# Performance work log

Hardware: AMD Instinct MI355X
Metric: run time of the kernel (lower is better)

## Reference

```python
import jax, jax.numpy as jnp
import numpy as np

DIM = 128
WIN = (2, 7, 7)
HEADS = 4
N = WIN[0] * WIN[1] * WIN[2]  # 98
B_ = 2048
NW = 256  # num windows per sample; B_ // NW = batch = 8


def _relative_position_index(win):
    t = np.arange(win[0]); h = np.arange(win[1]); w = np.arange(win[2])
    coords = np.stack(np.meshgrid(t, h, w, indexing='ij'))  # (3, T, H, W)
    cf = coords.reshape(3, -1)  # (3, N)
    rel = cf[:, :, None] - cf[:, None, :]  # (3, N, N)
    rel = rel.transpose(1, 2, 0).copy()
    rel[:, :, 0] += win[0] - 1
    rel[:, :, 1] += win[1] - 1
    rel[:, :, 2] += win[2] - 1
    rel[:, :, 0] *= (2 * win[1] - 1) * (2 * win[2] - 1)
    rel[:, :, 1] *= 2 * win[2] - 1
    return rel.sum(-1).astype(np.int32)  # (N, N)


def setup_inputs() -> dict:
    key = jax.random.key(0)
    ks = jax.random.split(key, 8)
    table_len = (2 * WIN[0] - 1) * (2 * WIN[1] - 1) * (2 * WIN[2] - 1)  # 507
    x = jax.random.normal(ks[0], (B_, N, DIM), dtype=jnp.float32)
    # 0 / -inf style additive mask (use -1e4 as finite -inf)
    u = jax.random.uniform(ks[1], (NW, N, N))
    mask = jnp.where(u < 0.9, 0.0, -1e4).astype(jnp.float32)
    qkv_w = jax.random.normal(ks[2], (3 * DIM, DIM), dtype=jnp.float32) * (DIM ** -0.5)
    qkv_b = jax.random.normal(ks[3], (3 * DIM,), dtype=jnp.float32) * 0.02
    proj_w = jax.random.normal(ks[4], (DIM, DIM), dtype=jnp.float32) * (DIM ** -0.5)
    proj_b = jax.random.normal(ks[5], (DIM,), dtype=jnp.float32) * 0.02
    bias_table = jax.random.normal(ks[6], (table_len, HEADS), dtype=jnp.float32) * 0.02
    rel_index = jnp.asarray(_relative_position_index(WIN))
    return {"x": x, "mask": mask, "qkv_w": qkv_w, "qkv_b": qkv_b,
            "proj_w": proj_w, "proj_b": proj_b, "bias_table": bias_table,
            "rel_index": rel_index}


def reference(x, mask, qkv_w, qkv_b, proj_w, proj_b, bias_table, rel_index):
    Bq, n, c = x.shape
    hd = c // HEADS
    scale = hd ** -0.5
    qkv = x @ qkv_w.T + qkv_b  # (B_, N, 3C)
    qkv = qkv.reshape(Bq, n, 3, HEADS, hd).transpose(2, 0, 3, 1, 4)  # (3, B_, H, N, hd)
    q, k, v = qkv[0] * scale, qkv[1], qkv[2]
    attn = jnp.einsum('bhnd,bhmd->bhnm', q, k)  # (B_, H, N, N)
    bias = bias_table[rel_index.reshape(-1)].reshape(n, n, HEADS)
    attn = attn + bias.transpose(2, 0, 1)[None]  # add (1, H, N, N)
    nW = mask.shape[0]
    attn = attn.reshape(Bq // nW, nW, HEADS, n, n) + mask[None, :, None]
    attn = jax.nn.softmax(attn.reshape(Bq, HEADS, n, n), axis=-1)
    out = jnp.einsum('bhnm,bhmd->bhnd', attn, v)  # (B_, H, N, hd)
    out = out.transpose(0, 2, 1, 3).reshape(Bq, n, c)
    return out @ proj_w.T + proj_b
```

## Files before the change

### kernel.cpp

```cpp
#include <hip/hip_runtime.h>
#include <hip/hip_bf16.h>


#define NTOK 98
#define NN (NTOK * NTOK)
#define SCALE 0.17677669529663687f
#define LOG2E 1.4426950408889634f

typedef short bf16x8 __attribute__((ext_vector_type(8)));
typedef float f32x4 __attribute__((ext_vector_type(4)));
#define MFMA(a, b, c) __builtin_amdgcn_mfma_f32_16x16x32_bf16(a, b, c, 0, 0, 0)

static __device__ __forceinline__ unsigned short f2bf(float f) {
  union { float f; unsigned int i; } x; x.f = f;
  unsigned int u = x.i;
  unsigned int rnd = ((u >> 16) & 1u) + 0x7fffu;
  return (unsigned short)((u + rnd) >> 16);
}

static __device__ __forceinline__ unsigned int cvt_pk_bf16(float lo, float hi) {
  unsigned int pk;
  asm("v_cvt_pk_bf16_f32 %0, %1, %2" : "=v"(pk) : "v"(lo), "v"(hi));
  return pk;
}

__global__ void k0_w(const float* __restrict__ qkv_w, const float* __restrict__ proj_w,
                     unsigned short* __restrict__ wqb, unsigned short* __restrict__ wpb) {
  int idx = blockIdx.x * 256 + threadIdx.x;
  if (idx < 49152) wqb[idx] = f2bf(qkv_w[idx]);
  else wpb[idx - 49152] = f2bf(proj_w[idx - 49152]);
}

__global__ void k0b_bm(const float* __restrict__ table, const int* __restrict__ rel,
                       const float* __restrict__ mask, unsigned int* __restrict__ bm) {
  const int wmodh = blockIdx.x, mt = blockIdx.y;
  const int wmod = wmodh >> 2, h = wmodh & 3;
  unsigned int* dst = bm + (size_t)(wmodh * 7 + mt) * 896;
  for (int u = threadIdx.x; u < 896; u += 256) {
    int w = u & 1, lane = (u >> 1) & 63, nt = u >> 7;
    int quad = lane >> 4, L15 = lane & 15;
    int col = nt * 16 + L15;
    unsigned int pk = 0;
#pragma unroll
    for (int rr = 0; rr < 2; ++rr) {
      int row = mt * 16 + quad * 4 + 2 * w + rr;
      float v = -1.0e30f;
      if (row < NTOK && col < NTOK) {
        int nm = row * NTOK + col;
        v = (table[rel[nm] * 4 + h] + mask[(size_t)wmod * NN + nm]) * LOG2E;
      }
      pk |= ((unsigned int)f2bf(v)) << (16 * rr);
    }
    dst[u] = pk;
  }
}

__global__ __launch_bounds__(256) void k1_qkv(const float* __restrict__ x,
                                              const unsigned short* __restrict__ wqb,
                                              const float* __restrict__ qkv_b,
                                              unsigned short* __restrict__ q,
                                              unsigned short* __restrict__ k,
                                              unsigned short* __restrict__ v) {
  __shared__ unsigned short xt[64 * 136];
  __shared__ unsigned short wt[128 * 136];
  const int t = threadIdx.x;
  const int r0 = blockIdx.x * 64;
  const int wv = t >> 6, lane = t & 63, L15 = lane & 15, quad = lane >> 4;

#pragma unroll
  for (int i = 0; i < 8; ++i) {
    int idx = t + (i << 8);
    int row = idx >> 5, c4 = idx & 31;
    float4 xv = *(const float4*)&x[(size_t)(r0 + row) * 128 + c4 * 4];
    ushort4 pk; pk.x = f2bf(xv.x); pk.y = f2bf(xv.y); pk.z = f2bf(xv.z); pk.w = f2bf(xv.w);
    *(ushort4*)&xt[row * 136 + c4 * 4] = pk;
  }

  bf16x8 af[4];
  bool afLoaded = false;

  for (int g = 0; g < 3; ++g) {
    if (g) __syncthreads();
#pragma unroll
    for (int i = 0; i < 8; ++i) {
      int idx = t + (i << 8);
      int c = idx >> 4, kq = idx & 15;
      *(uint4*)&wt[c * 136 + kq * 8] = ((const uint4*)wqb)[g * 2048 + idx];
    }
    __syncthreads();
    if (!afLoaded) {
      afLoaded = true;
#pragma unroll
      for (int kt = 0; kt < 4; ++kt)
        af[kt] = *(const bf16x8*)&xt[(wv * 16 + L15) * 136 + kt * 32 + quad * 8];
    }

    f32x4 acc[8];
#pragma unroll
    for (int nt = 0; nt < 8; ++nt) {
      f32x4 a = {0.f, 0.f, 0.f, 0.f};
#pragma unroll
      for (int kt = 0; kt < 4; ++kt) {
        bf16x8 bf_ = *(const bf16x8*)&wt[(nt * 16 + L15) * 136 + kt * 32 + quad * 8];
        a = MFMA(af[kt], bf_, a);
      }
      acc[nt] = a;
    }

    unsigned short* dst = (g == 0) ? q : ((g == 1) ? k : v);
    const float sc = (g == 0) ? (SCALE * LOG2E) : 1.0f;
    float bsc[8];
#pragma unroll
    for (int nt = 0; nt < 8; ++nt) bsc[nt] = qkv_b[g * 128 + nt * 16 + L15] * sc;
#pragma unroll
    for (int reg = 0; reg < 4; ++reg) {
      int R = r0 + wv * 16 + quad * 4 + reg;
      int b = R / NTOK, n = R - b * NTOK;
      size_t base0 = ((size_t)b * 4 * NTOK + n) * 32;
#pragma unroll
      for (int h2 = 0; h2 < 4; ++h2) {
        float v0 = acc[2 * h2][reg] * sc + bsc[2 * h2];
        float v1 = acc[2 * h2 + 1][reg] * sc + bsc[2 * h2 + 1];
        unsigned int pk = cvt_pk_bf16(v0, v1);
        unsigned short* dp = dst + base0 + (size_t)h2 * (NTOK * 32) + L15;
        dp[0]  = (unsigned short)pk;
        dp[16] = (unsigned short)(pk >> 16);
      }
    }
  }
}

__global__ __launch_bounds__(256, 4) void k2_attn(const unsigned short* __restrict__ qg,
                                                  const unsigned short* __restrict__ kg,
                                                  const unsigned short* __restrict__ vg,
                                                  const unsigned int* __restrict__ bm16,
                                                  unsigned short* __restrict__ og) {
  __shared__ unsigned short sK[112 * 40];
  __shared__ unsigned short sVt[32 * 136];
  __shared__ unsigned short sP[4 * 16 * 136];
  const int t = threadIdx.x;
  const int wmodh = blockIdx.x;
  const int wmod = wmodh >> 2, h = wmodh & 3;
  const int wv = t >> 6, lane = t & 63, L15 = lane & 15, quad = lane >> 4;
  unsigned short* myP = sP + wv * (16 * 136);

  for (int i = t; i < 280; i += 256) ((unsigned int*)sK)[1960 + i] = 0;
  for (int j = lane; j < 128; j += 64) {
    int r = j >> 3, cp = j & 7;
    *(unsigned int*)&myP[r * 136 + 112 + cp * 2] = 0;
  }
  for (int i = t; i < 32 * 30; i += 256) {
    int d = i / 30, nl = 98 + i % 30;
    int swz = ((d >> 3) & 3) << 3;
    sVt[d * 136 + (nl ^ swz)] = 0;
  }

  const int s0 = wv * 2, s1 = wv * 2 + 1;
  uint2 bmA[7], bmB[7];
  {
    const uint2* p0 = (const uint2*)(bm16 + (size_t)(wmodh * 7 + s0) * 896);
#pragma unroll
    for (int nt = 0; nt < 7; ++nt) bmA[nt] = p0[nt * 64 + lane];
    if (wv < 3) {
      const uint2* p1 = (const uint2*)(bm16 + (size_t)(wmodh * 7 + s1) * 896);
#pragma unroll
      for (int nt = 0; nt < 7; ++nt) bmB[nt] = p1[nt * 64 + lane];
    }
  }

  const int i0 = t, i1 = t + 256;
  uint4 rk0, rk1, rv0, rv1;
  auto loadKV = [&](int bh) {
    const uint4* kp = (const uint4*)kg + (size_t)bh * 392;
    const uint4* vp = (const uint4*)vg + (size_t)bh * 392;
    rk0 = kp[i0]; rv0 = vp[i0];
    if (i1 < 392) { rk1 = kp[i1]; rv1 = vp[i1]; }
  };
  loadKV(wmod * 4 + h);

  auto strip = [&](int mt, const uint2* bmp, bf16x8 aq, int bw) {
    f32x4 s[7];
#pragma unroll
    for (int nt = 0; nt < 7; ++nt) {
      uint2 pkb = bmp[nt];
      f32x4 c;
      c[0] = __uint_as_float(pkb.x << 16);
      c[1] = __uint_as_float(pkb.x & 0xffff0000u);
      c[2] = __uint_as_float(pkb.y << 16);
      c[3] = __uint_as_float(pkb.y & 0xffff0000u);
      bf16x8 bk = *(const bf16x8*)&sK[(nt * 16 + L15) * 40 + quad * 8];
      s[nt] = MFMA(aq, bk, c);
    }
    float rsv[4];
#pragma unroll
    for (int reg = 0; reg < 4; ++reg) {
      float sum = 0.f;
#pragma unroll
      for (int nt = 0; nt < 7; ++nt) {
        float e = __builtin_amdgcn_exp2f(s[nt][reg]);
        s[nt][reg] = e; sum += e;
      }
#pragma unroll
      for (int d = 1; d < 16; d <<= 1) sum += __shfl_xor(sum, d, 64);
      rsv[reg] = __builtin_amdgcn_rcpf(sum);
      unsigned short* pr = myP + (quad * 4 + reg) * 136 + L15;
#pragma unroll
      for (int p = 0; p < 4; ++p) {
        int n1 = (p < 3) ? 2 * p + 1 : 2 * p;
        unsigned int pk = cvt_pk_bf16(s[2 * p][reg], s[n1][reg]);
        pr[2 * p * 16] = (unsigned short)pk;
        if (p < 3) pr[n1 * 16] = (unsigned short)(pk >> 16);
      }
    }
    const int sw0 = (L15 >> 3) << 3;
    const int sw1 = (((16 + L15) >> 3) & 3) << 3;
    f32x4 o0 = {0.f, 0.f, 0.f, 0.f}, o1 = {0.f, 0.f, 0.f, 0.f};
#pragma unroll
    for (int kt = 0; kt < 4; ++kt) {
      int cb = kt * 32 + quad * 8;
      bf16x8 ap  = *(const bf16x8*)&myP[L15 * 136 + cb];
      bf16x8 bv0 = *(const bf16x8*)&sVt[L15 * 136 + (cb ^ sw0)];
      bf16x8 bv1 = *(const bf16x8*)&sVt[(16 + L15) * 136 + (cb ^ sw1)];
      o0 = MFMA(ap, bv0, o0);
      o1 = MFMA(ap, bv1, o1);
    }
#pragma unroll
    for (int reg = 0; reg < 4; ++reg) {
      int n = mt * 16 + quad * 4 + reg;
      if (n < NTOK) {
        size_t ob = ((size_t)bw * NTOK + n) * 128 + h * 32;
        float a0 = o0[reg] * rsv[reg], a1 = o1[reg] * rsv[reg];
        unsigned int pk = cvt_pk_bf16(a0, a1);
        og[ob + L15]      = (unsigned short)pk;
        og[ob + 16 + L15] = (unsigned short)(pk >> 16);
      }
    }
  };

  for (int it = 0; it < 8; ++it) {
    const int bw = wmod + (it << 8);
    const int bh = bw * 4 + h;
    const size_t base = (size_t)bh * (NTOK * 32);

    if (it) __syncthreads();
    {
      int row = i0 >> 2, kq = i0 & 3;
      *(uint4*)&sK[row * 40 + kq * 8] = rk0;
      int n = i0 >> 2, d0 = (i0 & 3) << 3;
      int swz = ((d0 >> 3) & 3) << 3;
      const unsigned short* pw = (const unsigned short*)&rv0;
#pragma unroll
      for (int j = 0; j < 8; ++j) sVt[(d0 + j) * 136 + (n ^ swz)] = pw[j];
      if (i1 < 392) {
        int row1 = i1 >> 2, kq1 = i1 & 3;
        *(uint4*)&sK[row1 * 40 + kq1 * 8] = rk1;
        int n_ = i1 >> 2, d0_ = (i1 & 3) << 3;
        int swz_ = ((d0_ >> 3) & 3) << 3;
        const unsigned short* pw1 = (const unsigned short*)&rv1;
#pragma unroll
        for (int j = 0; j < 8; ++j) sVt[(d0_ + j) * 136 + (n_ ^ swz_)] = pw1[j];
      }
    }
    __syncthreads();
    if (it < 7) loadKV((bw + 256) * 4 + h);

    bf16x8 aqA = *(const bf16x8*)&qg[base + (size_t)(s0 * 16 + L15) * 32 + quad * 8];
    bf16x8 aqB;
    if (wv < 3) aqB = *(const bf16x8*)&qg[base + (size_t)(s1 * 16 + L15) * 32 + quad * 8];

    strip(s0, bmA, aqA, bw);
    if (wv < 3) strip(s1, bmB, aqB, bw);
  }
}

__global__ __launch_bounds__(256) void k3_proj(const unsigned short* __restrict__ og,
                                               const unsigned short* __restrict__ wpb,
                                               const float* __restrict__ pb,
                                               float* __restrict__ out) {
  __shared__ unsigned short ot[64 * 136];
  __shared__ unsigned short wt[128 * 136];
  const int t = threadIdx.x;
  const int r0 = blockIdx.x * 64;
  const int wv = t >> 6, lane = t & 63, L15 = lane & 15, quad = lane >> 4;

#pragma unroll
  for (int i = 0; i < 4; ++i) {
    int idx = t + (i << 8);
    int row = idx >> 4, kq = idx & 15;
    *(uint4*)&ot[row * 136 + kq * 8] = ((const uint4*)og)[(size_t)(r0 + row) * 16 + kq];
  }
#pragma unroll
  for (int i = 0; i < 8; ++i) {
    int idx = t + (i << 8);
    int c = idx >> 4, kq = idx & 15;
    *(uint4*)&wt[c * 136 + kq * 8] = ((const uint4*)wpb)[idx];
  }
  __syncthreads();

  bf16x8 af[4];
#pragma unroll
  for (int kt = 0; kt < 4; ++kt)
    af[kt] = *(const bf16x8*)&ot[(wv * 16 + L15) * 136 + kt * 32 + quad * 8];

  f32x4 acc[8];
#pragma unroll
  for (int nt = 0; nt < 8; ++nt) {
    f32x4 a = {0.f, 0.f, 0.f, 0.f};
#pragma unroll
    for (int kt = 0; kt < 4; ++kt) {
      bf16x8 bf_ = *(const bf16x8*)&wt[(nt * 16 + L15) * 136 + kt * 32 + quad * 8];
      a = MFMA(af[kt], bf_, a);
    }
    acc[nt] = a;
  }

  float bias[8];
#pragma unroll
  for (int nt = 0; nt < 8; ++nt) bias[nt] = pb[nt * 16 + L15];
#pragma unroll
  for (int reg = 0; reg < 4; ++reg) {
    size_t R = (size_t)(r0 + wv * 16 + quad * 4 + reg);
#pragma unroll
    for (int nt = 0; nt < 8; ++nt)
      out[R * 128 + nt * 16 + L15] = acc[nt][reg] + bias[nt];
  }
}

extern "C" void kernel_launch(void* const* d_in, const int* in_sizes, int n_in,
                              void* d_out, int out_size, void* d_ws, size_t ws_size,
                              hipStream_t stream) {
  (void)in_sizes; (void)n_in; (void)out_size; (void)ws_size;
  const float* x      = (const float*)d_in[0];
  const float* mask   = (const float*)d_in[1];
  const float* qkv_w  = (const float*)d_in[2];
  const float* qkv_b  = (const float*)d_in[3];
  const float* proj_w = (const float*)d_in[4];
  const float* proj_b = (const float*)d_in[5];
  const float* table  = (const float*)d_in[6];
  const int*   rel    = (const int*)d_in[7];
  float* out = (float*)d_out;

  const size_t QS = (size_t)2048 * 4 * NTOK * 32;
  unsigned short* q   = (unsigned short*)d_ws;
  unsigned short* k   = q + QS;
  unsigned short* v   = k + QS;
  unsigned short* o   = v + QS;
  unsigned short* wqb = o + QS;
  unsigned short* wpb = wqb + 49152;
  unsigned int* bm = (unsigned int*)d_out;

  k0_w<<<256, 256, 0, stream>>>(qkv_w, proj_w, wqb, wpb);
  k0b_bm<<<dim3(1024, 7), 256, 0, stream>>>(table, rel, mask, bm);
  k1_qkv<<<200704 / 64, 256, 0, stream>>>(x, wqb, qkv_b, q, k, v);
  k2_attn<<<1024, 256, 0, stream>>>(q, k, v, bm, o);
  k3_proj<<<200704 / 64, 256, 0, stream>>>(o, wpb, proj_b, out);
}
```

Baseline: 370.9 us.

## Pack bf16 pairs into 32-bit stores via permuted head-dim layout, prefetch Q, add setprio

Changes the head-dim layout of q/k/v and the attention output so adjacent head-dim pairs (d, d+16) are stored as one 32-bit word. The proj weight columns are permuted at conversion time to match, which replaces pairs of 16-bit global stores with single 32-bit stores. The V transpose into LDS is rewritten to unpack the new interleaved layout. Q fragments for the next iteration are prefetched alongside K/V, and MFMA sections are wrapped in s_setprio to favour matrix issue across waves.

```diff
diff --git a/kernel.cpp b/kernel.cpp
--- a/kernel.cpp
+++ b/kernel.cpp
@@ -27,8 +27,14 @@
 __global__ void k0_w(const float* __restrict__ qkv_w, const float* __restrict__ proj_w,
                      unsigned short* __restrict__ wqb, unsigned short* __restrict__ wpb) {
   int idx = blockIdx.x * 256 + threadIdx.x;
-  if (idx < 49152) wqb[idx] = f2bf(qkv_w[idx]);
-  else wpb[idx - 49152] = f2bf(proj_w[idx - 49152]);
+  if (idx < 49152) {
+    wqb[idx] = f2bf(qkv_w[idx]);
+  } else {
+    int m2 = idx - 49152;
+    int m = m2 & 127;
+    int pim = (m & ~31) | ((m & 1) << 4) | ((m & 31) >> 1);
+    wpb[m2] = f2bf(proj_w[(m2 & ~127) | pim]);
+  }
 }
 
 __global__ void k0b_bm(const float* __restrict__ table, const int* __restrict__ rel,
@@ -72,8 +78,8 @@
     int idx = t + (i << 8);
     int row = idx >> 5, c4 = idx & 31;
     float4 xv = *(const float4*)&x[(size_t)(r0 + row) * 128 + c4 * 4];
-    ushort4 pk; pk.x = f2bf(xv.x); pk.y = f2bf(xv.y); pk.z = f2bf(xv.z); pk.w = f2bf(xv.w);
-    *(ushort4*)&xt[row * 136 + c4 * 4] = pk;
+    uint2 pk; pk.x = cvt_pk_bf16(xv.x, xv.y); pk.y = cvt_pk_bf16(xv.z, xv.w);
+    *(uint2*)&xt[row * 136 + c4 * 4] = pk;
   }
 
   bf16x8 af[4];
@@ -107,7 +113,7 @@
       acc[nt] = a;
     }
 
-    unsigned short* dst = (g == 0) ? q : ((g == 1) ? k : v);
+    unsigned int* dst32 = (unsigned int*)((g == 0) ? q : ((g == 1) ? k : v));
     const float sc = (g == 0) ? (SCALE * LOG2E) : 1.0f;
     float bsc[8];
 #pragma unroll
@@ -116,15 +122,12 @@
     for (int reg = 0; reg < 4; ++reg) {
       int R = r0 + wv * 16 + quad * 4 + reg;
       int b = R / NTOK, n = R - b * NTOK;
-      size_t base0 = ((size_t)b * 4 * NTOK + n) * 32;
+      size_t base32 = ((size_t)b * 4 * NTOK + n) * 16;
 #pragma unroll
       for (int h2 = 0; h2 < 4; ++h2) {
         float v0 = acc[2 * h2][reg] * sc + bsc[2 * h2];
         float v1 = acc[2 * h2 + 1][reg] * sc + bsc[2 * h2 + 1];
-        unsigned int pk = cvt_pk_bf16(v0, v1);
-        unsigned short* dp = dst + base0 + (size_t)h2 * (NTOK * 32) + L15;
-        dp[0]  = (unsigned short)pk;
-        dp[16] = (unsigned short)(pk >> 16);
+        dst32[base32 + (size_t)h2 * (NTOK * 16) + L15] = cvt_pk_bf16(v0, v1);
       }
     }
   }
@@ -176,10 +179,18 @@
     rk0 = kp[i0]; rv0 = vp[i0];
     if (i1 < 392) { rk1 = kp[i1]; rv1 = vp[i1]; }
   };
+  bf16x8 qA0, qB0, qA1, qB1;
+  auto loadQ = [&](int bh, bf16x8& qa, bf16x8& qb) {
+    const size_t base = (size_t)bh * (NTOK * 32);
+    qa = *(const bf16x8*)&qg[base + (size_t)(s0 * 16 + L15) * 32 + quad * 8];
+    if (wv < 3) qb = *(const bf16x8*)&qg[base + (size_t)(s1 * 16 + L15) * 32 + quad * 8];
+  };
   loadKV(wmod * 4 + h);
+  loadQ(wmod * 4 + h, qA0, qB0);
 
   auto strip = [&](int mt, const uint2* bmp, bf16x8 aq, int bw) {
     f32x4 s[7];
+    __builtin_amdgcn_s_setprio(1);
 #pragma unroll
     for (int nt = 0; nt < 7; ++nt) {
       uint2 pkb = bmp[nt];
@@ -191,6 +202,7 @@
       bf16x8 bk = *(const bf16x8*)&sK[(nt * 16 + L15) * 40 + quad * 8];
       s[nt] = MFMA(aq, bk, c);
     }
+    __builtin_amdgcn_s_setprio(0);
     float rsv[4];
 #pragma unroll
     for (int reg = 0; reg < 4; ++reg) {
@@ -215,6 +227,7 @@
     const int sw0 = (L15 >> 3) << 3;
     const int sw1 = (((16 + L15) >> 3) & 3) << 3;
     f32x4 o0 = {0.f, 0.f, 0.f, 0.f}, o1 = {0.f, 0.f, 0.f, 0.f};
+    __builtin_amdgcn_s_setprio(1);
 #pragma unroll
     for (int kt = 0; kt < 4; ++kt) {
       int cb = kt * 32 + quad * 8;
@@ -224,52 +237,56 @@
       o0 = MFMA(ap, bv0, o0);
       o1 = MFMA(ap, bv1, o1);
     }
+    __builtin_amdgcn_s_setprio(0);
 #pragma unroll
     for (int reg = 0; reg < 4; ++reg) {
       int n = mt * 16 + quad * 4 + reg;
       if (n < NTOK) {
-        size_t ob = ((size_t)bw * NTOK + n) * 128 + h * 32;
         float a0 = o0[reg] * rsv[reg], a1 = o1[reg] * rsv[reg];
-        unsigned int pk = cvt_pk_bf16(a0, a1);
-        og[ob + L15]      = (unsigned short)pk;
-        og[ob + 16 + L15] = (unsigned short)(pk >> 16);
+        ((unsigned int*)og)[(size_t)(bw * NTOK + n) * 64 + h * 16 + L15] =
+            cvt_pk_bf16(a0, a1);
       }
     }
   };
 
   for (int it = 0; it < 8; ++it) {
     const int bw = wmod + (it << 8);
-    const int bh = bw * 4 + h;
-    const size_t base = (size_t)bh * (NTOK * 32);
 
     if (it) __syncthreads();
     {
       int row = i0 >> 2, kq = i0 & 3;
       *(uint4*)&sK[row * 40 + kq * 8] = rk0;
-      int n = i0 >> 2, d0 = (i0 & 3) << 3;
-      int swz = ((d0 >> 3) & 3) << 3;
-      const unsigned short* pw = (const unsigned short*)&rv0;
-#pragma unroll
-      for (int j = 0; j < 8; ++j) sVt[(d0 + j) * 136 + (n ^ swz)] = pw[j];
+      int n = i0 >> 2, j0 = (i0 & 3) << 2;
+      const unsigned int* pw = (const unsigned int*)&rv0;
+#pragma unroll
+      for (int j = 0; j < 4; ++j) {
+        int dlo = j0 + j, dhi = dlo + 16;
+        sVt[dlo * 136 + (n ^ (((dlo >> 3) & 3) << 3))] = (unsigned short)pw[j];
+        sVt[dhi * 136 + (n ^ (((dhi >> 3) & 3) << 3))] = (unsigned short)(pw[j] >> 16);
+      }
       if (i1 < 392) {
         int row1 = i1 >> 2, kq1 = i1 & 3;
         *(uint4*)&sK[row1 * 40 + kq1 * 8] = rk1;
-        int n_ = i1 >> 2, d0_ = (i1 & 3) << 3;
-        int swz_ = ((d0_ >> 3) & 3) << 3;
-        const unsigned short* pw1 = (const unsigned short*)&rv1;
-#pragma unroll
-        for (int j = 0; j < 8; ++j) sVt[(d0_ + j) * 136 + (n_ ^ swz_)] = pw1[j];
+        int n_ = i1 >> 2, j0_ = (i1 & 3) << 2;
+        const unsigned int* pw1 = (const unsigned int*)&rv1;
+#pragma unroll
+        for (int j = 0; j < 4; ++j) {
+          int dlo = j0_ + j, dhi = dlo + 16;
+          sVt[dlo * 136 + (n_ ^ (((dlo >> 3) & 3) << 3))] = (unsigned short)pw1[j];
+          sVt[dhi * 136 + (n_ ^ (((dhi >> 3) & 3) << 3))] = (unsigned short)(pw1[j] >> 16);
+        }
       }
     }
     __syncthreads();
-    if (it < 7) loadKV((bw + 256) * 4 + h);
-
-    bf16x8 aqA = *(const bf16x8*)&qg[base + (size_t)(s0 * 16 + L15) * 32 + quad * 8];
-    bf16x8 aqB;
-    if (wv < 3) aqB = *(const bf16x8*)&qg[base + (size_t)(s1 * 16 + L15) * 32 + quad * 8];
-
-    strip(s0, bmA, aqA, bw);
-    if (wv < 3) strip(s1, bmB, aqB, bw);
+    if (it < 7) {
+      int bhn = (bw + 256) * 4 + h;
+      loadKV(bhn);
+      loadQ(bhn, qA1, qB1);
+    }
+
+    strip(s0, bmA, qA0, bw);
+    if (wv < 3) strip(s1, bmB, qB0, bw);
+    qA0 = qA1; qB0 = qB1;
   }
 }
 
```

Measured after the change: 379.9 us. +2.4%, slower.
